# Performance work log

Hardware: AMD Instinct MI355X
Metric: run time of the kernel (lower is better)

Reference implementation:

```python
import jax, jax.numpy as jnp
import numpy as np

HEADS = 8
DIM_HEAD = 128
EPS = 1e-5


def layer_norm(t, gamma):
    mu = jnp.mean(t, axis=-1, keepdims=True)
    var = jnp.var(t, axis=-1, keepdims=True)
    return (t - mu) / jnp.sqrt(var + EPS) * gamma


def setup_inputs() -> dict:
    key = jax.random.key(0)
    k1, k2, k3 = jax.random.split(key, 3)
    B, N, T, D = 16, 256, 4096, 1024
    img_queries = jax.random.normal(k1, (B, N, D), dtype=jnp.float32)
    x = jax.random.normal(k2, (B, T, D), dtype=jnp.float32)
    gamma_q = jnp.ones((D,), dtype=jnp.float32)
    gamma_x = jnp.ones((D,), dtype=jnp.float32)
    W_kv = jax.random.normal(k3, (D, 2 * DIM_HEAD), dtype=jnp.float32) * 0.02
    return {"img_queries": img_queries, "x": x, "gamma_q": gamma_q,
            "gamma_x": gamma_x, "W_kv": W_kv}


def reference(img_queries, x, gamma_q, gamma_x, W_kv):
    B, N, D = img_queries.shape
    scale = DIM_HEAD ** -0.5
    q_n = layer_norm(img_queries, gamma_q)            # [B,N,D]
    x_n = layer_norm(x, gamma_x)                      # [B,T,D]
    # b n (h d) -> b h n d
    q = q_n.reshape(B, N, HEADS, DIM_HEAD).transpose(0, 2, 1, 3)
    kv = x_n @ W_kv                                   # [B,T,2*dim_head]
    k = kv[..., :DIM_HEAD]                            # shared single K head; v chunk unused
    sim = jnp.einsum('bhid,bjd->bhij', q * scale, k)  # [B,H,N,T]
    sim = sim - jnp.max(sim, axis=-1, keepdims=True)
    attn = jax.nn.softmax(sim, axis=-1)
    out = jnp.einsum('bhij,bjf->bhif', attn, x_n)     # V = raw normed x, [B,H,N,D]
    # b h n f -> b (n h f)
    out = out.transpose(0, 2, 1, 3).reshape(B, N * HEADS * D)
    return out, attn
```

## Files before the change

kernel.cpp:

```cpp
#include <hip/hip_runtime.h>

typedef unsigned short u16;
typedef unsigned int u32;
typedef __attribute__((ext_vector_type(8))) short short8;
typedef __attribute__((ext_vector_type(4))) float f32x4;
typedef __attribute__((ext_vector_type(4))) unsigned int u32x4;

#define SCALE 0.08838834764831845f
#define OUT_ELEMS 33554432ull

__device__ __forceinline__ u16 f2b(float f) {
  u32 u = __float_as_uint(f);
  u32 r = u + 0x7fffu + ((u >> 16) & 1u);
  return (u16)(r >> 16);
}

__device__ __forceinline__ u32 cvtpk(float lo, float hi) {
  u32 r;
  asm("v_cvt_pk_bf16_f32 %0, %1, %2" : "=v"(r) : "v"(lo), "v"(hi));
  return r;
}

__device__ __forceinline__ void gload16(const void* g, void* l) {
  __builtin_amdgcn_global_load_lds((const __attribute__((address_space(1))) void*)g,
                                   (__attribute__((address_space(3))) void*)l, 16, 0, 0);
}

__device__ __forceinline__ uint2 shflx2(uint2 v, int m) {
  uint2 r;
  r.x = __shfl_xor(v.x, m, 64);
  r.y = __shfl_xor(v.y, m, 64);
  return r;
}

__global__ __launch_bounds__(256) void ln_rows(const float* __restrict__ in,
                                               const float* __restrict__ gamma,
                                               u16* __restrict__ out, float scale) {
  const int row = blockIdx.x;
  const int t = threadIdx.x;
  const float4 v = *(const float4*)(in + (size_t)row * 1024 + t * 4);
  float s = v.x + v.y + v.z + v.w;
  float q = v.x * v.x + v.y * v.y + v.z * v.z + v.w * v.w;
#pragma unroll
  for (int m = 32; m; m >>= 1) {
    s += __shfl_down(s, m);
    q += __shfl_down(q, m);
  }
  __shared__ float red[8];
  const int w = t >> 6;
  if ((t & 63) == 0) { red[w] = s; red[4 + w] = q; }
  __syncthreads();
  s = red[0] + red[1] + red[2] + red[3];
  q = red[4] + red[5] + red[6] + red[7];
  const float mu = s * (1.0f / 1024.0f);
  const float var = q * (1.0f / 1024.0f) - mu * mu;
  const float rs = rsqrtf(var + 1e-5f) * scale;
  const float4 g = *(const float4*)(gamma + t * 4);
  ushort4 o;
  o.x = f2b((v.x - mu) * rs * g.x);
  o.y = f2b((v.y - mu) * rs * g.y);
  o.z = f2b((v.z - mu) * rs * g.z);
  o.w = f2b((v.w - mu) * rs * g.w);
  *(ushort4*)(out + (size_t)row * 1024 + t * 4) = o;
}

__global__ __launch_bounds__(1024) void ln_xpose(const float* __restrict__ in,
                                                 const float* __restrict__ gamma,
                                                 u16* __restrict__ xn,
                                                 u16* __restrict__ xnt) {
  __shared__ u16 tile[32][1024];
  const int blk = blockIdx.x;
  const int b = blk >> 7;
  const int jj0 = (blk & 127) * 32;
  const int t = threadIdx.x;
  const int lane = t & 63, w = t >> 6;
  const size_t j0 = (size_t)blk * 32;

  float4 gv[4];
#pragma unroll
  for (int k = 0; k < 4; ++k) gv[k] = *(const float4*)(gamma + k * 256 + lane * 4);

  float4 va[2][4];
  float mu[2], rs[2];
#pragma unroll
  for (int rr = 0; rr < 2; ++rr) {
    const int row = w * 2 + rr;
    const float* src = in + (j0 + row) * 1024;
    float s = 0.f, q = 0.f;
#pragma unroll
    for (int k = 0; k < 4; ++k) {
      const float4 v = *(const float4*)(src + k * 256 + lane * 4);
      va[rr][k] = v;
      s += v.x + v.y + v.z + v.w;
      q += v.x * v.x + v.y * v.y + v.z * v.z + v.w * v.w;
    }
#pragma unroll
    for (int m = 1; m < 64; m <<= 1) {
      s += __shfl_xor(s, m);
      q += __shfl_xor(q, m);
    }
    const float m_ = s * (1.0f / 1024.0f);
    mu[rr] = m_;
    rs[rr] = rsqrtf(q * (1.0f / 1024.0f) - m_ * m_ + 1e-5f);
  }
#pragma unroll
  for (int rr = 0; rr < 2; ++rr) {
    const int row = w * 2 + rr;
    u16* xrow = xn + (j0 + row) * 1024;
#pragma unroll
    for (int k = 0; k < 4; ++k) {
      const float4 v = va[rr][k];
      uint2 p;
      p.x = cvtpk((v.x - mu[rr]) * rs[rr] * gv[k].x, (v.y - mu[rr]) * rs[rr] * gv[k].y);
      p.y = cvtpk((v.z - mu[rr]) * rs[rr] * gv[k].z, (v.w - mu[rr]) * rs[rr] * gv[k].w);
      *(uint2*)(xrow + k * 256 + lane * 4) = p;
      *(uint2*)(&tile[row][k * 256 + lane * 4]) = p;
    }
  }
  __syncthreads();
  u32 o[16];
#pragma unroll
  for (int r = 0; r < 16; ++r)
    o[r] = (u32)tile[2 * r][t] | ((u32)tile[2 * r + 1][t] << 16);
  u16* dst = xnt + ((size_t)b * 1024 + t) * 4096 + jj0;
#pragma unroll
  for (int k = 0; k < 4; ++k) {
    u32x4 v = {o[4 * k + 0], o[4 * k + 1], o[4 * k + 2], o[4 * k + 3]};
    *(u32x4*)(dst + k * 8) = v;
  }
}

__global__ __launch_bounds__(256) void cvt_w(const float* __restrict__ w, u16* __restrict__ wt) {
  const int n = blockIdx.x;
  const int t = threadIdx.x;
  const int d = t * 4;
  ushort4 o;
  o.x = f2b(w[(size_t)(d + 0) * 256 + n]);
  o.y = f2b(w[(size_t)(d + 1) * 256 + n]);
  o.z = f2b(w[(size_t)(d + 2) * 256 + n]);
  o.w = f2b(w[(size_t)(d + 3) * 256 + n]);
  *(ushort4*)(wt + (size_t)n * 1024 + d) = o;
}

__global__ __launch_bounds__(256) void kgemm(const u16* __restrict__ xn,
                                             const u16* __restrict__ wt,
                                             u16* __restrict__ ks) {
  __shared__ u16 As[128 * 32];
  __shared__ u16 Bs[128 * 32];
  const int t = threadIdx.x;
  const int lane = t & 63, w = t >> 6;
  const int wm = w >> 1, wn = w & 1;
  const int j0 = blockIdx.x * 128;
  const int g = lane >> 4, r16 = lane & 15;
  f32x4 acc[4][4] = {};
  for (int k0 = 0; k0 < 1024; k0 += 32) {
    __syncthreads();
#pragma unroll
    for (int i = 0; i < 2; ++i) {
      const int seg = i * 4 + w;
      const int off = seg * 1024 + lane * 16;
      const int row = off >> 6;
      const int c = (off >> 4) & 3;
      const int sw = c ^ ((row >> 1) & 3);
      gload16(xn + ((size_t)(j0 + row)) * 1024 + k0 + sw * 8, (char*)As + seg * 1024);
      gload16(wt + ((size_t)row) * 1024 + k0 + sw * 8, (char*)Bs + seg * 1024);
    }
    __syncthreads();
    short8 a[4], bq[4];
#pragma unroll
    for (int mt = 0; mt < 4; ++mt) {
      const int row = wm * 64 + mt * 16 + r16;
      const int sw = g ^ ((row >> 1) & 3);
      a[mt] = *(const short8*)(As + row * 32 + sw * 8);
    }
#pragma unroll
    for (int nt = 0; nt < 4; ++nt) {
      const int row = wn * 64 + nt * 16 + r16;
      const int sw = g ^ ((row >> 1) & 3);
      bq[nt] = *(const short8*)(Bs + row * 32 + sw * 8);
    }
#pragma unroll
    for (int mt = 0; mt < 4; ++mt)
#pragma unroll
      for (int nt = 0; nt < 4; ++nt)
        acc[mt][nt] = __builtin_amdgcn_mfma_f32_16x16x32_bf16(a[mt], bq[nt], acc[mt][nt], 0, 0, 0);
  }
#pragma unroll
  for (int mt = 0; mt < 4; ++mt)
#pragma unroll
    for (int nt = 0; nt < 4; ++nt)
#pragma unroll
      for (int r = 0; r < 4; ++r) {
        const int j = j0 + wm * 64 + mt * 16 + g * 4 + r;
        const int n = wn * 64 + nt * 16 + r16;
        ks[(size_t)j * 128 + n] = f2b(acc[mt][nt][r]);
      }
}

__global__ __launch_bounds__(1024) void attn_kernel(const u16* __restrict__ qs,
                                                    const u16* __restrict__ ks,
                                                    u16* __restrict__ attnb) {
  const int orig = blockIdx.x;
  const int blk = (orig & 7) * 256 + (orig >> 3);
  const int it = blk & 15, h = (blk >> 4) & 7, b = blk >> 7;
  const int i0 = it * 16;
  const int t = threadIdx.x;
  const int lane = t & 63, w = t >> 6;
  const int g = lane >> 4, r16 = lane & 15;
  __shared__ u16 Q[16 * 128];
  __shared__ float redm[256];
  __shared__ float reds[256];
  if (t < 256) {
    const int row = t >> 4, c = t & 15;
    const int sw = c ^ (row & 7);
    *(short8*)(Q + row * 128 + sw * 8) =
        *(const short8*)(qs + ((size_t)(b * 256 + i0 + row)) * 1024 + h * 128 + c * 8);
  }
  __syncthreads();
  short8 a[4];
#pragma unroll
  for (int kp = 0; kp < 4; ++kp) {
    const int c = kp * 4 + g;
    const int sw = c ^ (r16 & 7);
    a[kp] = *(const short8*)(Q + r16 * 128 + sw * 8);
  }
  const u16* kb = ks + (size_t)b * 4096 * 128;
  const int j0 = w * 256;
  f32x4 acc[16] = {};
#pragma unroll
  for (int kp = 0; kp < 4; ++kp) {
#pragma unroll
    for (int nt = 0; nt < 16; ++nt) {
      const short8 bv = *(const short8*)(kb + (size_t)(j0 + nt * 16 + r16) * 128 + kp * 32 + g * 8);
      acc[nt] = __builtin_amdgcn_mfma_f32_16x16x32_bf16(bv, a[kp], acc[nt], 0, 0, 0);
    }
  }
  float mx = acc[0][0];
#pragma unroll
  for (int nt = 0; nt < 16; ++nt)
#pragma unroll
    for (int r = 0; r < 4; ++r) mx = fmaxf(mx, acc[nt][r]);
  mx = fmaxf(mx, __shfl_xor(mx, 16));
  mx = fmaxf(mx, __shfl_xor(mx, 32));
  float sm = 0.f;
#pragma unroll
  for (int nt = 0; nt < 16; ++nt)
#pragma unroll
    for (int r = 0; r < 4; ++r) {
      const float p = __expf(acc[nt][r] - mx);
      acc[nt][r] = p;
      sm += p;
    }
  sm += __shfl_xor(sm, 16);
  sm += __shfl_xor(sm, 32);
  if (lane < 16) {
    redm[w * 16 + lane] = mx;
    reds[w * 16 + lane] = sm;
  }
  __syncthreads();
  float m = redm[r16];
#pragma unroll
  for (int w2 = 1; w2 < 16; ++w2) m = fmaxf(m, redm[w2 * 16 + r16]);
  float s = 0.f;
#pragma unroll
  for (int w2 = 0; w2 < 16; ++w2)
    s += reds[w2 * 16 + r16] * __expf(redm[w2 * 16 + r16] - m);
  const float f = __expf(mx - m) / s;
#pragma unroll
  for (int nt = 0; nt < 16; ++nt) acc[nt] *= f;

  u16* brow = attnb + ((size_t)((b * 8 + h) * 256 + i0 + r16)) * 4096 + j0;
  const bool gb0 = (g & 1), gb1 = (g & 2);
#pragma unroll
  for (int q4 = 0; q4 < 4; ++q4) {
    uint2 X[4];
#pragma unroll
    for (int i = 0; i < 4; ++i) {
      const f32x4 v = acc[q4 * 4 + i];
      X[i] = make_uint2(cvtpk(v[0], v[1]), cvtpk(v[2], v[3]));
    }
#pragma unroll
    for (int k = 0; k < 2; ++k) {
      const uint2 aa = X[2 * k], bb = X[2 * k + 1];
      const uint2 sent = gb0 ? aa : bb;
      const uint2 recv = shflx2(sent, 16);
      X[2 * k] = gb0 ? recv : aa;
      X[2 * k + 1] = gb0 ? bb : recv;
    }
#pragma unroll
    for (int k = 0; k < 2; ++k) {
      const uint2 aa = X[k], bb = X[k + 2];
      const uint2 sent = gb1 ? aa : bb;
      const uint2 recv = shflx2(sent, 32);
      X[k] = gb1 ? recv : aa;
      X[k + 2] = gb1 ? bb : recv;
    }
    u16* bp = brow + q4 * 64 + g * 16;
    u32x4 o0 = {X[0].x, X[0].y, X[1].x, X[1].y};
    u32x4 o1 = {X[2].x, X[2].y, X[3].x, X[3].y};
    *(u32x4*)bp = o0;
    *(u32x4*)(bp + 8) = o1;
  }
}

__global__ __launch_bounds__(512, 2) void ogemm256(const u16* __restrict__ attnb,
                                                   const u16* __restrict__ xnt,
                                                   float* __restrict__ out,
                                                   float* __restrict__ attn) {
  extern __shared__ u16 S[];
  const int orig = blockIdx.x;
  const int wid = (orig & 7) * 64 + (orig >> 3);
  const int b = wid >> 5, ft = (wid >> 3) & 3, h = wid & 7;
  const int t = threadIdx.x;
  const int lane = t & 63, w = t >> 6;
  const int wm = w >> 2, wn = w & 3;
  const int g = lane >> 4, r16 = lane & 15;
  const u16* Ab = attnb + ((size_t)(b * 8 + h) * 256) * 4096;
  const u16* Bb = xnt + ((size_t)b * 1024 + ft * 256) * 4096;
  const bool wrA = (ft == 0);
  float* attn_out = attn + ((size_t)(b * 8 + h) * 256) * 4096;
  const int wr_base = w * 4 + (lane >> 4);
  const int wc16 = lane & 15;
  const int wchunk = wc16 >> 1;
  const int whalf = (wc16 & 1) * 8;

  int srow[4], scol[4];
#pragma unroll
  for (int seg = 0; seg < 4; ++seg) {
    const int gi = seg * 512 + t;
    srow[seg] = gi >> 3;
    scol[seg] = (((gi & 7) ^ ((gi >> 3) & 7)) * 8);
  }
  const int wuni = w * 1024;

#define OSTAGE(buf, k0)                                                         \
  do {                                                                          \
    _Pragma("unroll") for (int seg = 0; seg < 4; ++seg)                         \
        gload16(Ab + (size_t)srow[seg] * 4096 + (k0) + scol[seg],               \
                (char*)S + (buf)*32768 + seg * 8192 + wuni);                    \
    _Pragma("unroll") for (int seg = 0; seg < 4; ++seg)                         \
        gload16(Bb + (size_t)srow[seg] * 4096 + (k0) + scol[seg],               \
                (char*)S + 65536 + (buf)*32768 + seg * 8192 + wuni);            \
  } while (0)

  f32x4 acc[8][4] = {};
  OSTAGE(0, 0);
  OSTAGE(1, 64);
  asm volatile("s_waitcnt vmcnt(8)" ::: "memory");
  __builtin_amdgcn_s_barrier();

  for (int t64 = 0; t64 < 64; ++t64) {
    const int buf = t64 & 1;
    const char* A0 = (const char*)S + buf * 32768;
    const char* B0 = (const char*)S + 65536 + buf * 32768;
    short8 af[8], bf[4];
#pragma unroll
    for (int mt = 0; mt < 8; ++mt) {
      const int row = wm * 128 + mt * 16 + r16;
      af[mt] = *(const short8*)(A0 + row * 128 + ((g ^ (row & 7)) * 16));
    }
#pragma unroll
    for (int nt = 0; nt < 4; ++nt) {
      const int row = wn * 64 + nt * 16 + r16;
      bf[nt] = *(const short8*)(B0 + row * 128 + ((g ^ (row & 7)) * 16));
    }
    asm volatile("s_waitcnt lgkmcnt(0)" ::: "memory");
    __builtin_amdgcn_sched_barrier(0);
    __builtin_amdgcn_s_setprio(1);
#pragma unroll
    for (int mt = 0; mt < 8; ++mt)
#pragma unroll
      for (int nt = 0; nt < 4; ++nt)
        acc[mt][nt] = __builtin_amdgcn_mfma_f32_16x16x32_bf16(af[mt], bf[nt], acc[mt][nt], 0, 0, 0);
    __builtin_amdgcn_s_setprio(0);
#pragma unroll
    for (int mt = 0; mt < 8; ++mt) {
      const int row = wm * 128 + mt * 16 + r16;
      af[mt] = *(const short8*)(A0 + row * 128 + (((4 + g) ^ (row & 7)) * 16));
    }
#pragma unroll
    for (int nt = 0; nt < 4; ++nt) {
      const int row = wn * 64 + nt * 16 + r16;
      bf[nt] = *(const short8*)(B0 + row * 128 + (((4 + g) ^ (row & 7)) * 16));
    }
    uint2 wv[8];
    if (wrA) {
#pragma unroll
      for (int s = 0; s < 8; ++s) {
        const int row = s * 32 + wr_base;
        wv[s] = *(const uint2*)(A0 + row * 128 + ((wchunk ^ (row & 7)) * 16) + whalf);
      }
    }
    asm volatile("s_waitcnt lgkmcnt(0)" ::: "memory");
    __builtin_amdgcn_sched_barrier(0);
    if (wrA) {
#pragma unroll
      for (int s = 0; s < 8; ++s) {
        const int row = s * 32 + wr_base;
        f32x4 o;
        o[0] = __uint_as_float(wv[s].x << 16);
        o[1] = __uint_as_float(wv[s].x & 0xffff0000u);
        o[2] = __uint_as_float(wv[s].y << 16);
        o[3] = __uint_as_float(wv[s].y & 0xffff0000u);
        __builtin_nontemporal_store(o, (f32x4*)(attn_out + (size_t)row * 4096 + t64 * 64 + wc16 * 4));
      }
      __builtin_amdgcn_sched_barrier(0);
    }
    __builtin_amdgcn_s_barrier();
    if (t64 + 2 < 64) OSTAGE(buf, (t64 + 2) * 64);
    __builtin_amdgcn_s_setprio(1);
#pragma unroll
    for (int mt = 0; mt < 8; ++mt)
#pragma unroll
      for (int nt = 0; nt < 4; ++nt)
        acc[mt][nt] = __builtin_amdgcn_mfma_f32_16x16x32_bf16(af[mt], bf[nt], acc[mt][nt], 0, 0, 0);
    __builtin_amdgcn_s_setprio(0);
    if (t64 + 2 < 64) {
      if (wrA)
        asm volatile("s_waitcnt vmcnt(16)" ::: "memory");
      else
        asm volatile("s_waitcnt vmcnt(8)" ::: "memory");
    } else if (t64 == 62) {
      asm volatile("s_waitcnt vmcnt(0)" ::: "memory");
    }
    __builtin_amdgcn_s_barrier();
  }
#undef OSTAGE

  float* ob = out + (size_t)b * 2097152 + (size_t)h * 1024;
#pragma unroll
  for (int mt = 0; mt < 8; ++mt)
#pragma unroll
    for (int nt = 0; nt < 4; ++nt)
#pragma unroll
      for (int r = 0; r < 4; ++r) {
        const int i = wm * 128 + mt * 16 + g * 4 + r;
        const int f = ft * 256 + wn * 64 + nt * 16 + r16;
        ob[(size_t)i * 8192 + f] = acc[mt][nt][r];
      }
}

extern "C" void kernel_launch(void* const* d_in, const int* in_sizes, int n_in,
                              void* d_out, int out_size, void* d_ws, size_t ws_size,
                              hipStream_t stream) {
  const float* img_q = (const float*)d_in[0];
  const float* x = (const float*)d_in[1];
  const float* gamma_q = (const float*)d_in[2];
  const float* gamma_x = (const float*)d_in[3];
  const float* wkv = (const float*)d_in[4];

  float* out_f = (float*)d_out;
  float* attn_f = out_f + OUT_ELEMS;

  u16* xn = (u16*)attn_f;
  u16* qsb = (u16*)out_f;
  u16* wtb = qsb + 4194304;
  u16* ksb = wtb + 131072;
  u16* xnt = (u16*)d_ws;
  u16* attnb = xnt + 67108864;

  if (ws_size < (size_t)402653184) return;

  (void)hipFuncSetAttribute((const void*)ogemm256,
                            hipFuncAttributeMaxDynamicSharedMemorySize, 131072);

  ln_xpose<<<2048, 1024, 0, stream>>>(x, gamma_x, xn, xnt);
  ln_rows<<<4096, 256, 0, stream>>>(img_q, gamma_q, qsb, SCALE);
  cvt_w<<<128, 256, 0, stream>>>(wkv, wtb);
  kgemm<<<512, 256, 0, stream>>>(xn, wtb, ksb);
  attn_kernel<<<2048, 1024, 0, stream>>>(qsb, ksb, attnb);
  ogemm256<<<512, 512, 131072, stream>>>(attnb, xnt, out_f, attn_f);
}
```

Measured before the change: 817.0 us.

## Fuse K projection GEMM into LayerNorm-transpose kernel using LDS tile

The separate kgemm kernel is removed. The K = x_n·W_k projection is now computed inside the LayerNorm/transpose kernel from the normalized bf16 tile already held in LDS, so the row-major xn buffer no longer needs to be written and read back. The LDS tile gains an XOR swizzle so that both the transpose reads and the MFMA A-fragment reads avoid bank conflicts. In exchange, each block reads its W_k fragments straight from global memory without LDS staging, and cvt_w must now run before the fused kernel.

```diff
diff --git a/kernel.cpp b/kernel.cpp
--- a/kernel.cpp
+++ b/kernel.cpp
@@ -64,72 +64,6 @@
   *(ushort4*)(out + (size_t)row * 1024 + t * 4) = o;
 }
 
-__global__ __launch_bounds__(1024) void ln_xpose(const float* __restrict__ in,
-                                                 const float* __restrict__ gamma,
-                                                 u16* __restrict__ xn,
-                                                 u16* __restrict__ xnt) {
-  __shared__ u16 tile[32][1024];
-  const int blk = blockIdx.x;
-  const int b = blk >> 7;
-  const int jj0 = (blk & 127) * 32;
-  const int t = threadIdx.x;
-  const int lane = t & 63, w = t >> 6;
-  const size_t j0 = (size_t)blk * 32;
-
-  float4 gv[4];
-#pragma unroll
-  for (int k = 0; k < 4; ++k) gv[k] = *(const float4*)(gamma + k * 256 + lane * 4);
-
-  float4 va[2][4];
-  float mu[2], rs[2];
-#pragma unroll
-  for (int rr = 0; rr < 2; ++rr) {
-    const int row = w * 2 + rr;
-    const float* src = in + (j0 + row) * 1024;
-    float s = 0.f, q = 0.f;
-#pragma unroll
-    for (int k = 0; k < 4; ++k) {
-      const float4 v = *(const float4*)(src + k * 256 + lane * 4);
-      va[rr][k] = v;
-      s += v.x + v.y + v.z + v.w;
-      q += v.x * v.x + v.y * v.y + v.z * v.z + v.w * v.w;
-    }
-#pragma unroll
-    for (int m = 1; m < 64; m <<= 1) {
-      s += __shfl_xor(s, m);
-      q += __shfl_xor(q, m);
-    }
-    const float m_ = s * (1.0f / 1024.0f);
-    mu[rr] = m_;
-    rs[rr] = rsqrtf(q * (1.0f / 1024.0f) - m_ * m_ + 1e-5f);
-  }
-#pragma unroll
-  for (int rr = 0; rr < 2; ++rr) {
-    const int row = w * 2 + rr;
-    u16* xrow = xn + (j0 + row) * 1024;
-#pragma unroll
-    for (int k = 0; k < 4; ++k) {
-      const float4 v = va[rr][k];
-      uint2 p;
-      p.x = cvtpk((v.x - mu[rr]) * rs[rr] * gv[k].x, (v.y - mu[rr]) * rs[rr] * gv[k].y);
-      p.y = cvtpk((v.z - mu[rr]) * rs[rr] * gv[k].z, (v.w - mu[rr]) * rs[rr] * gv[k].w);
-      *(uint2*)(xrow + k * 256 + lane * 4) = p;
-      *(uint2*)(&tile[row][k * 256 + lane * 4]) = p;
-    }
-  }
-  __syncthreads();
-  u32 o[16];
-#pragma unroll
-  for (int r = 0; r < 16; ++r)
-    o[r] = (u32)tile[2 * r][t] | ((u32)tile[2 * r + 1][t] << 16);
-  u16* dst = xnt + ((size_t)b * 1024 + t) * 4096 + jj0;
-#pragma unroll
-  for (int k = 0; k < 4; ++k) {
-    u32x4 v = {o[4 * k + 0], o[4 * k + 1], o[4 * k + 2], o[4 * k + 3]};
-    *(u32x4*)(dst + k * 8) = v;
-  }
-}
-
 __global__ __launch_bounds__(256) void cvt_w(const float* __restrict__ w, u16* __restrict__ wt) {
   const int n = blockIdx.x;
   const int t = threadIdx.x;
@@ -142,59 +76,96 @@
   *(ushort4*)(wt + (size_t)n * 1024 + d) = o;
 }
 
-__global__ __launch_bounds__(256) void kgemm(const u16* __restrict__ xn,
-                                             const u16* __restrict__ wt,
-                                             u16* __restrict__ ks) {
-  __shared__ u16 As[128 * 32];
-  __shared__ u16 Bs[128 * 32];
+__global__ __launch_bounds__(1024) void ln_xpose_k(const float* __restrict__ in,
+                                                   const float* __restrict__ gamma,
+                                                   const u16* __restrict__ wt,
+                                                   u16* __restrict__ xnt,
+                                                   u16* __restrict__ ks) {
+  __shared__ u16 tile[32][1024];
+  const int blk = blockIdx.x;
+  const int b = blk >> 7;
+  const int jj0 = (blk & 127) * 32;
   const int t = threadIdx.x;
   const int lane = t & 63, w = t >> 6;
-  const int wm = w >> 1, wn = w & 1;
-  const int j0 = blockIdx.x * 128;
-  const int g = lane >> 4, r16 = lane & 15;
-  f32x4 acc[4][4] = {};
-  for (int k0 = 0; k0 < 1024; k0 += 32) {
-    __syncthreads();
-#pragma unroll
-    for (int i = 0; i < 2; ++i) {
-      const int seg = i * 4 + w;
-      const int off = seg * 1024 + lane * 16;
-      const int row = off >> 6;
-      const int c = (off >> 4) & 3;
-      const int sw = c ^ ((row >> 1) & 3);
-      gload16(xn + ((size_t)(j0 + row)) * 1024 + k0 + sw * 8, (char*)As + seg * 1024);
-      gload16(wt + ((size_t)row) * 1024 + k0 + sw * 8, (char*)Bs + seg * 1024);
-    }
-    __syncthreads();
-    short8 a[4], bq[4];
-#pragma unroll
-    for (int mt = 0; mt < 4; ++mt) {
-      const int row = wm * 64 + mt * 16 + r16;
-      const int sw = g ^ ((row >> 1) & 3);
-      a[mt] = *(const short8*)(As + row * 32 + sw * 8);
-    }
-#pragma unroll
-    for (int nt = 0; nt < 4; ++nt) {
-      const int row = wn * 64 + nt * 16 + r16;
-      const int sw = g ^ ((row >> 1) & 3);
-      bq[nt] = *(const short8*)(Bs + row * 32 + sw * 8);
-    }
-#pragma unroll
-    for (int mt = 0; mt < 4; ++mt)
-#pragma unroll
-      for (int nt = 0; nt < 4; ++nt)
-        acc[mt][nt] = __builtin_amdgcn_mfma_f32_16x16x32_bf16(a[mt], bq[nt], acc[mt][nt], 0, 0, 0);
-  }
-#pragma unroll
-  for (int mt = 0; mt < 4; ++mt)
-#pragma unroll
-    for (int nt = 0; nt < 4; ++nt)
-#pragma unroll
-      for (int r = 0; r < 4; ++r) {
-        const int j = j0 + wm * 64 + mt * 16 + g * 4 + r;
-        const int n = wn * 64 + nt * 16 + r16;
-        ks[(size_t)j * 128 + n] = f2b(acc[mt][nt][r]);
-      }
+  const size_t j0 = (size_t)blk * 32;
+
+  float4 gv[4];
+#pragma unroll
+  for (int k = 0; k < 4; ++k) gv[k] = *(const float4*)(gamma + k * 256 + lane * 4);
+
+  float4 va[2][4];
+  float mu[2], rs[2];
+#pragma unroll
+  for (int rr = 0; rr < 2; ++rr) {
+    const int row = w * 2 + rr;
+    const float* src = in + (j0 + row) * 1024;
+    float s = 0.f, q = 0.f;
+#pragma unroll
+    for (int k = 0; k < 4; ++k) {
+      const float4 v = *(const float4*)(src + k * 256 + lane * 4);
+      va[rr][k] = v;
+      s += v.x + v.y + v.z + v.w;
+      q += v.x * v.x + v.y * v.y + v.z * v.z + v.w * v.w;
+    }
+#pragma unroll
+    for (int m = 1; m < 64; m <<= 1) {
+      s += __shfl_xor(s, m);
+      q += __shfl_xor(q, m);
+    }
+    const float m_ = s * (1.0f / 1024.0f);
+    mu[rr] = m_;
+    rs[rr] = rsqrtf(q * (1.0f / 1024.0f) - m_ * m_ + 1e-5f);
+  }
+#pragma unroll
+  for (int rr = 0; rr < 2; ++rr) {
+    const int row = w * 2 + rr;
+#pragma unroll
+    for (int k = 0; k < 4; ++k) {
+      const float4 v = va[rr][k];
+      uint2 p;
+      p.x = cvtpk((v.x - mu[rr]) * rs[rr] * gv[k].x, (v.y - mu[rr]) * rs[rr] * gv[k].y);
+      p.y = cvtpk((v.z - mu[rr]) * rs[rr] * gv[k].z, (v.w - mu[rr]) * rs[rr] * gv[k].w);
+      const int chunk = k * 32 + (lane >> 1);
+      const int cs = (chunk & 0x78) | ((chunk ^ row) & 7);
+      *(uint2*)(&tile[row][cs * 8 + (lane & 1) * 4]) = p;
+    }
+  }
+  __syncthreads();
+  {
+    const int ct = t >> 3, wt8 = t & 7;
+    u32 o[16];
+#pragma unroll
+    for (int r = 0; r < 16; ++r) {
+      const int c0 = (ct & 0x78) | ((ct ^ (2 * r)) & 7);
+      const int c1 = (ct & 0x78) | ((ct ^ (2 * r + 1)) & 7);
+      o[r] = (u32)tile[2 * r][c0 * 8 + wt8] | ((u32)tile[2 * r + 1][c1 * 8 + wt8] << 16);
+    }
+    u16* dst = xnt + ((size_t)b * 1024 + t) * 4096 + jj0;
+#pragma unroll
+    for (int k = 0; k < 4; ++k) {
+      u32x4 v = {o[4 * k + 0], o[4 * k + 1], o[4 * k + 2], o[4 * k + 3]};
+      *(u32x4*)(dst + k * 8) = v;
+    }
+  }
+  {
+    const int wm = w >> 3, wn = w & 7;
+    const int g = lane >> 4, r16 = lane & 15;
+    const int arow = wm * 16 + r16;
+    f32x4 acc = {};
+#pragma unroll
+    for (int kp = 0; kp < 32; ++kp) {
+      const int chunk = kp * 4 + g;
+      const int cs = (chunk & 0x78) | ((chunk ^ arow) & 7);
+      const short8 a = *(const short8*)(&tile[arow][cs * 8]);
+      const short8 bf = *(const short8*)(wt + (size_t)(wn * 16 + r16) * 1024 + kp * 32 + g * 8);
+      acc = __builtin_amdgcn_mfma_f32_16x16x32_bf16(a, bf, acc, 0, 0, 0);
+    }
+#pragma unroll
+    for (int r = 0; r < 4; ++r) {
+      const size_t j = j0 + wm * 16 + g * 4 + r;
+      ks[j * 128 + wn * 16 + r16] = f2b(acc[r]);
+    }
+  }
 }
 
 __global__ __launch_bounds__(1024) void attn_kernel(const u16* __restrict__ qs,
@@ -452,7 +423,6 @@
   float* out_f = (float*)d_out;
   float* attn_f = out_f + OUT_ELEMS;
 
-  u16* xn = (u16*)attn_f;
   u16* qsb = (u16*)out_f;
   u16* wtb = qsb + 4194304;
   u16* ksb = wtb + 131072;
@@ -464,10 +434,9 @@
   (void)hipFuncSetAttribute((const void*)ogemm256,
                             hipFuncAttributeMaxDynamicSharedMemorySize, 131072);
 
-  ln_xpose<<<2048, 1024, 0, stream>>>(x, gamma_x, xn, xnt);
+  cvt_w<<<128, 256, 0, stream>>>(wkv, wtb);
   ln_rows<<<4096, 256, 0, stream>>>(img_q, gamma_q, qsb, SCALE);
-  cvt_w<<<128, 256, 0, stream>>>(wkv, wtb);
-  kgemm<<<512, 256, 0, stream>>>(xn, wtb, ksb);
+  ln_xpose_k<<<2048, 1024, 0, stream>>>(x, gamma_x, wtb, xnt, ksb);
   attn_kernel<<<2048, 1024, 0, stream>>>(qsb, ksb, attnb);
   ogemm256<<<512, 512, 131072, stream>>>(attnb, xnt, out_f, attn_f);
 }
```

New measurement: 864.2 us. +5.8%, slower.

## Spread fp32 attn write-out evenly across all four feature-tile blocks

Applied to the files above, without the earlier changes.

Previously only the ft==0 block of each (b,h) wrote the fp32 attention matrix, so it did 8 row-segments of stores per K step while the other three blocks wrote nothing. Now each of the four ft blocks writes a 64-row quarter of the staged attn tile, one 16-byte LDS read and two 16-byte nontemporal stores per thread per step. The vmcnt wait becomes a single uniform value. This balances store traffic and removes the straggler block, at the cost of every block now issuing stores during its main loop.

```diff
diff --git a/kernel.cpp b/kernel.cpp
--- a/kernel.cpp
+++ b/kernel.cpp
@@ -317,12 +317,9 @@
   const int g = lane >> 4, r16 = lane & 15;
   const u16* Ab = attnb + ((size_t)(b * 8 + h) * 256) * 4096;
   const u16* Bb = xnt + ((size_t)b * 1024 + ft * 256) * 4096;
-  const bool wrA = (ft == 0);
-  float* attn_out = attn + ((size_t)(b * 8 + h) * 256) * 4096;
-  const int wr_base = w * 4 + (lane >> 4);
-  const int wc16 = lane & 15;
-  const int wchunk = wc16 >> 1;
-  const int whalf = (wc16 & 1) * 8;
+  const int wrow = ft * 64 + (t >> 3);
+  const int wci = t & 7;
+  float* wdst = attn + ((size_t)(b * 8 + h) * 256 + wrow) * 4096 + wci * 8;
 
   int srow[4], scol[4];
 #pragma unroll
@@ -383,27 +380,19 @@
       const int row = wn * 64 + nt * 16 + r16;
       bf[nt] = *(const short8*)(B0 + row * 128 + (((4 + g) ^ (row & 7)) * 16));
     }
-    uint2 wv[8];
-    if (wrA) {
-#pragma unroll
-      for (int s = 0; s < 8; ++s) {
-        const int row = s * 32 + wr_base;
-        wv[s] = *(const uint2*)(A0 + row * 128 + ((wchunk ^ (row & 7)) * 16) + whalf);
-      }
-    }
+    const short8 wv = *(const short8*)(A0 + wrow * 128 + ((wci ^ (wrow & 7)) * 16));
     asm volatile("s_waitcnt lgkmcnt(0)" ::: "memory");
     __builtin_amdgcn_sched_barrier(0);
-    if (wrA) {
-#pragma unroll
-      for (int s = 0; s < 8; ++s) {
-        const int row = s * 32 + wr_base;
-        f32x4 o;
-        o[0] = __uint_as_float(wv[s].x << 16);
-        o[1] = __uint_as_float(wv[s].x & 0xffff0000u);
-        o[2] = __uint_as_float(wv[s].y << 16);
-        o[3] = __uint_as_float(wv[s].y & 0xffff0000u);
-        __builtin_nontemporal_store(o, (f32x4*)(attn_out + (size_t)row * 4096 + t64 * 64 + wc16 * 4));
+    {
+      f32x4 lo, hi;
+#pragma unroll
+      for (int e = 0; e < 4; ++e) {
+        lo[e] = __uint_as_float(((u32)(u16)wv[e]) << 16);
+        hi[e] = __uint_as_float(((u32)(u16)wv[4 + e]) << 16);
       }
+      float* dst = wdst + t64 * 64;
+      __builtin_nontemporal_store(lo, (f32x4*)dst);
+      __builtin_nontemporal_store(hi, (f32x4*)(dst + 4));
       __builtin_amdgcn_sched_barrier(0);
     }
     __builtin_amdgcn_s_barrier();
@@ -416,10 +405,7 @@
         acc[mt][nt] = __builtin_amdgcn_mfma_f32_16x16x32_bf16(af[mt], bf[nt], acc[mt][nt], 0, 0, 0);
     __builtin_amdgcn_s_setprio(0);
     if (t64 + 2 < 64) {
-      if (wrA)
-        asm volatile("s_waitcnt vmcnt(16)" ::: "memory");
-      else
-        asm volatile("s_waitcnt vmcnt(8)" ::: "memory");
+      asm volatile("s_waitcnt vmcnt(10)" ::: "memory");
     } else if (t64 == 62) {
       asm volatile("s_waitcnt vmcnt(0)" ::: "memory");
     }
```

New measurement: 817.7 us. About the same (+0.1%).
